# Kernel tuning notes

Hardware: AMD Instinct MI355X
Metric: run time of the kernel (lower is better)

## Reference

```python
import jax, jax.numpy as jnp
import numpy as np

HORIZON = 20
DT = 0.1
EPS = 1e-4
V_MAX = 0.22
W_MAX = 2.8
BATCH = 1048576


def _inv_softplus(v):
    # matches StaticDifferentiableLQR._positive_inverse_softplus
    v = np.clip(np.asarray(v, np.float32) - EPS, 1e-6, None)
    return np.log(np.expm1(v)).astype(np.float32)


def setup_inputs() -> dict:
    key = jax.random.key(0)
    ref = jax.random.normal(key, (BATCH, 5), dtype=jnp.float32)
    return {
        "reference": ref,
        "q_raw": jnp.asarray(_inv_softplus([2.0, 6.0, 4.0])),
        "r_raw": jnp.asarray(_inv_softplus([0.5, 0.8])),
        "qf_raw": jnp.asarray(_inv_softplus([4.0, 10.0, 6.0])),
    }


def _lqr_forward(ref, q_raw, r_raw, qf_raw):
    dtype = ref.dtype
    bsz = ref.shape[0]
    error = ref[:, 0:3]          # [B,3]
    u_ref = ref[:, 3:5]          # [B,2]
    v_ref = u_ref[:, 0]
    w_ref = u_ref[:, 1]

    dt = jnp.asarray(DT, dtype)
    z = jnp.zeros_like(v_ref)
    one = jnp.ones_like(v_ref)
    # Linearized unicycle dynamics A:[B,3,3], B:[B,3,2]
    A = jnp.stack([
        jnp.stack([one, dt * w_ref, z], axis=-1),
        jnp.stack([-dt * w_ref, one, dt * v_ref], axis=-1),
        jnp.stack([z, z, one], axis=-1),
    ], axis=1)
    Bm = jnp.zeros((bsz, 3, 2), dtype).at[:, 0, 0].set(-dt).at[:, 2, 1].set(-dt)

    q = jax.nn.softplus(q_raw) + EPS
    r = jax.nn.softplus(r_raw) + EPS
    qf = jax.nn.softplus(qf_raw) + EPS
    Q = jnp.diag(q).astype(dtype)        # [3,3], broadcasts over batch
    R = jnp.diag(r).astype(dtype)        # [2,2]
    P0 = jnp.broadcast_to(jnp.diag(qf).astype(dtype), (bsz, 3, 3))
    I2 = jnp.eye(2, dtype=dtype)
    K_init = jnp.zeros((bsz, 2, 3), dtype)

    def riccati_step(carry, _):
        P, _ = carry
        BtP = jnp.einsum('bji,bjk->bik', Bm, P)          # B^T P  [B,2,3]
        S = R + BtP @ Bm + EPS * I2                       # [B,2,2]
        K = jnp.linalg.solve(S, BtP @ A)                  # [B,2,3]
        AtP = jnp.einsum('bji,bjk->bik', A, P)            # A^T P  [B,3,3]
        # Q + A^T P A - A^T P B K == Q + A^T P (A - B K)
        P_new = Q + AtP @ (A - Bm @ K)
        return (P_new, K), None

    (_, K0), _ = jax.lax.scan(riccati_step, (P0, K_init), None, length=HORIZON)

    delta_u = -jnp.einsum('bij,bj->bi', K0, error)        # [B,2]
    mean = u_ref + delta_u
    v = jnp.clip(mean[:, 0], -V_MAX, V_MAX)
    w = jnp.clip(mean[:, 1], -W_MAX, W_MAX)
    return jnp.stack([v, w], axis=-1)


def reference(reference, q_raw, r_raw, qf_raw):
    return _lqr_forward(reference, q_raw, r_raw, qf_raw)
```

## Files before the change

### kernel.cpp

```cpp
#include <hip/hip_runtime.h>
#include <math.h>

#define HORIZON 20
#define DT      0.1f
#define EPS     1e-4f
#define V_MAX   0.22f
#define W_MAX   2.8f

#define NQ     57
#define NODES  (NQ * NQ)
#define QHI    4.0f
#define INV_H  ((float)(NQ - 1) / QHI)

#define CAP      65536
#define LIST_OFF 64
#define TBL_OFF  262144

typedef _Float16 h2 __attribute__((ext_vector_type(2)));

__device__ __forceinline__ float softplus_f(float x) {
    return fmaxf(x, 0.0f) + log1pf(expf(-fabsf(x)));
}

__device__ void riccati_K(
    float vref, float wref,
    const float* __restrict__ q_raw, const float* __restrict__ r_raw,
    const float* __restrict__ qf_raw, float K[6])
{
    const float q0  = softplus_f(q_raw[0])  + EPS;
    const float q1  = softplus_f(q_raw[1])  + EPS;
    const float q2  = softplus_f(q_raw[2])  + EPS;
    const float r0e = softplus_f(r_raw[0])  + EPS + EPS;
    const float r1e = softplus_f(r_raw[1])  + EPS + EPS;
    const float qf0 = softplus_f(qf_raw[0]) + EPS;
    const float qf1 = softplus_f(qf_raw[1]) + EPS;
    const float qf2 = softplus_f(qf_raw[2]) + EPS;

    const float dt  = DT;
    const float dt2 = dt * dt;
    const float dtw = dt * wref;
    const float dtv = dt * vref;

    float p00 = qf0, p01 = 0.f, p02 = 0.f, p11 = qf1, p12 = 0.f, p22 = qf2;
    float k00 = 0.f, k01 = 0.f, k02 = 0.f, k10 = 0.f, k11 = 0.f, k12 = 0.f;

    #pragma unroll
    for (int t = 0; t < HORIZON; ++t) {
        const float t00 = p00 - dtw * p01;
        const float t01 = p01 - dtw * p11;
        const float t02 = p02 - dtw * p12;
        const float t10 = dtw * p00 + p01;
        const float t11 = dtw * p01 + p11;
        const float t12 = dtw * p02 + p12;
        const float t20 = dtv * p01 + p02;
        const float t21 = dtv * p11 + p12;
        const float t22 = dtv * p12 + p22;

        const float s00 = r0e + dt2 * p00;
        const float s01 =       dt2 * p02;
        const float s11 = r1e + dt2 * p22;
        const float c = -dt * __builtin_amdgcn_rcpf(s00 * s11 - s01 * s01);
        const float cs11 = c * s11, cs01 = c * s01, cs00 = c * s00;

        k00 = cs11 * t00 - cs01 * t02;
        k01 = cs11 * t10 - cs01 * t12;
        k02 = cs11 * t20 - cs01 * t22;
        k10 = cs00 * t02 - cs01 * t00;
        k11 = cs00 * t12 - cs01 * t10;
        k12 = cs00 * t22 - cs01 * t20;

        const float a00 = 1.0f + dt * k00;
        const float a01 = dtw  + dt * k01;
        const float a02 =        dt * k02;
        const float a20 =        dt * k10;
        const float a21 =        dt * k11;
        const float a22 = 1.0f + dt * k12;

        p00 = q0 + t00 * a00 - t01 * dtw + t02 * a20;
        p01 =      t00 * a01 + t01       + t02 * a21;
        p02 =      t00 * a02 + t01 * dtv + t02 * a22;
        p11 = q1 + t10 * a01 + t11       + t12 * a21;
        p12 =      t10 * a02 + t11 * dtv + t12 * a22;
        p22 = q2 + t20 * a02 + t21 * dtv + t22 * a22;
    }
    K[0] = k00; K[1] = k01; K[2] = k02;
    K[3] = k10; K[4] = k11; K[5] = k12;
}

__device__ __forceinline__ unsigned pack2(float a, float b) {
    h2 h; h[0] = (_Float16)a; h[1] = (_Float16)b;
    return __builtin_bit_cast(unsigned, h);
}

__global__ __launch_bounds__(256) void table_kernel(
    const float* __restrict__ q_raw, const float* __restrict__ r_raw,
    const float* __restrict__ qf_raw, unsigned* __restrict__ ws)
{
    const int idx = blockIdx.x * blockDim.x + threadIdx.x;
    if (idx == 0) ws[0] = 0u;
    if (idx >= NODES) return;
    const int iv = idx % NQ;
    const int iw = idx / NQ;
    const float v = (QHI / (float)(NQ - 1)) * (float)iv;
    const float w = (QHI / (float)(NQ - 1)) * (float)iw;
    float K[6];
    riccati_K(v, w, q_raw, r_raw, qf_raw, K);
    uint4* tbl = reinterpret_cast<uint4*>(ws + TBL_OFF);
    tbl[idx] = make_uint4(pack2(K[0], K[1]), pack2(K[2], K[3]),
                          pack2(K[4], K[5]), 0u);
}

__device__ __forceinline__ float2 eval_one(
    const uint4* __restrict__ nodes,
    float e0, float e1, float e2, float vref, float wref, bool* oor)
{
    const float s1 = (wref < 0.0f) ? -1.0f : 1.0f;
    const float v1 = s1 * vref, w1 = s1 * wref;
    const float e1f = s1 * e1;
    const float s2 = (v1 < 0.0f) ? -1.0f : 1.0f;
    const float vq = s2 * v1;
    const float e2f = s2 * e2;

    *oor = (vq > QHI) | (w1 > QHI);

    float fv = fminf(vq * INV_H, (float)(NQ - 1) - 1e-3f);
    float fw = fminf(w1 * INV_H, (float)(NQ - 1) - 1e-3f);
    const int iv = (int)fv;  const float av = fv - (float)iv;
    const int iw = (int)fw;  const float aw = fw - (float)iw;
    const int b = iw * NQ + iv;

    const uint4 A = nodes[b],      B = nodes[b + 1];
    const uint4 C = nodes[b + NQ], D = nodes[b + NQ + 1];

    const _Float16 hu00 = (_Float16)((1.0f - av) * (1.0f - aw));
    const _Float16 hu01 = (_Float16)(av * (1.0f - aw));
    const _Float16 hu10 = (_Float16)((1.0f - av) * aw);
    const _Float16 hu11 = (_Float16)(av * aw);
    const h2 W00 = {hu00, hu00}, W01 = {hu01, hu01},
             W10 = {hu10, hu10}, W11 = {hu11, hu11};

    #define H2(u) __builtin_bit_cast(h2, u)
    h2 r0 = W00 * H2(A.x) + W01 * H2(B.x) + W10 * H2(C.x) + W11 * H2(D.x);
    h2 r1 = W00 * H2(A.y) + W01 * H2(B.y) + W10 * H2(C.y) + W11 * H2(D.y);
    h2 r2 = W00 * H2(A.z) + W01 * H2(B.z) + W10 * H2(C.z) + W11 * H2(D.z);
    #undef H2

    const float k0 = (float)r0[0], k1 = (float)r0[1];
    const float k2 = (float)r1[0], k3 = (float)r1[1];
    const float k4 = (float)r2[0], k5 = (float)r2[1];

    const float du0 =       k0 * e0 + k1 * e1f + k2 * e2f;
    const float du1 = s2 * (k3 * e0 + k4 * e1f + k5 * e2f);
    const float v = fminf(fmaxf(vref - du0, -V_MAX), V_MAX);
    const float w = fminf(fmaxf(wref - du1, -W_MAX), W_MAX);
    return make_float2(v, w);
}

__global__ __launch_bounds__(512, 4) void lqr_main(
    const float* __restrict__ ref,
    unsigned* __restrict__ ws,
    float* __restrict__ out,
    int batch)
{
    __shared__ uint4 lds[NODES];
    const uint4* gt = reinterpret_cast<const uint4*>(ws + TBL_OFF);
    for (int j = threadIdx.x; j < NODES; j += 512)
        lds[j] = gt[j];
    __syncthreads();

    const int t    = blockIdx.x * 512 + threadIdx.x;
    const int base = 4 * t;
    if (base >= batch) return;

    unsigned* cnt  = ws;
    unsigned* list = ws + LIST_OFF;

    if (base + 3 < batch) {
        const float4* r4 = reinterpret_cast<const float4*>(ref + 5 * base);
        const float4 d0 = r4[0], d1 = r4[1], d2 = r4[2], d3 = r4[3], d4 = r4[4];
        const float r[20] = {d0.x,d0.y,d0.z,d0.w, d1.x,d1.y,d1.z,d1.w,
                             d2.x,d2.y,d2.z,d2.w, d3.x,d3.y,d3.z,d3.w,
                             d4.x,d4.y,d4.z,d4.w};
        bool o0, o1, o2, o3;
        const float2 c0 = eval_one(lds, r[0], r[1], r[2], r[3], r[4], &o0);
        const float2 c1 = eval_one(lds, r[5], r[6], r[7], r[8], r[9], &o1);
        const float2 c2 = eval_one(lds, r[10],r[11],r[12],r[13],r[14], &o2);
        const float2 c3 = eval_one(lds, r[15],r[16],r[17],r[18],r[19], &o3);

        float4* o4 = reinterpret_cast<float4*>(out + 2 * base);
        o4[0] = make_float4(c0.x, c0.y, c1.x, c1.y);
        o4[1] = make_float4(c2.x, c2.y, c3.x, c3.y);

        if (o0) { unsigned p = atomicAdd(cnt, 1u); if (p < CAP) list[p] = base;     }
        if (o1) { unsigned p = atomicAdd(cnt, 1u); if (p < CAP) list[p] = base + 1; }
        if (o2) { unsigned p = atomicAdd(cnt, 1u); if (p < CAP) list[p] = base + 2; }
        if (o3) { unsigned p = atomicAdd(cnt, 1u); if (p < CAP) list[p] = base + 3; }
    } else {
        for (int k = 0; k < 4 && base + k < batch; ++k) {
            const float* r = ref + 5 * (base + k);
            bool oo;
            const float2 c = eval_one(lds, r[0], r[1], r[2], r[3], r[4], &oo);
            out[2 * (base + k)]     = c.x;
            out[2 * (base + k) + 1] = c.y;
            if (oo) { unsigned p = atomicAdd(cnt, 1u); if (p < CAP) list[p] = base + k; }
        }
    }
}

__global__ __launch_bounds__(256) void fixup_kernel(
    const float* __restrict__ ref,
    const unsigned* __restrict__ ws,
    const float* __restrict__ q_raw, const float* __restrict__ r_raw,
    const float* __restrict__ qf_raw,
    float* __restrict__ out)
{
    const unsigned n = min(ws[0], (unsigned)CAP);
    const unsigned* list = ws + LIST_OFF;
    for (unsigned j = threadIdx.x; j < n; j += 256) {
        const unsigned idx = list[j];
        const float e0 = ref[5*idx], e1 = ref[5*idx+1], e2 = ref[5*idx+2];
        const float vr = ref[5*idx+3], wr = ref[5*idx+4];
        float K[6];
        riccati_K(vr, wr, q_raw, r_raw, qf_raw, K);
        const float du0 = K[0]*e0 + K[1]*e1 + K[2]*e2;
        const float du1 = K[3]*e0 + K[4]*e1 + K[5]*e2;
        out[2*idx]   = fminf(fmaxf(vr - du0, -V_MAX), V_MAX);
        out[2*idx+1] = fminf(fmaxf(wr - du1, -W_MAX), W_MAX);
    }
}

extern "C" void kernel_launch(void* const* d_in, const int* in_sizes, int n_in,
                              void* d_out, int out_size, void* d_ws, size_t ws_size,
                              hipStream_t stream) {
    const float* ref    = (const float*)d_in[0];
    const float* q_raw  = (const float*)d_in[1];
    const float* r_raw  = (const float*)d_in[2];
    const float* qf_raw = (const float*)d_in[3];
    float* out = (float*)d_out;
    unsigned* ws = (unsigned*)d_ws;

    const int batch = in_sizes[0] / 5;
    const int quads = (batch + 3) / 4;

    table_kernel<<<(NODES + 255) / 256, 256, 0, stream>>>(q_raw, r_raw, qf_raw, ws);

    const int grid = (quads + 511) / 512;
    lqr_main<<<grid, 512, 0, stream>>>(ref, ws, out, batch);

    fixup_kernel<<<1, 256, 0, stream>>>(ref, ws, q_raw, r_raw, qf_raw, out);
}
```

Measured before the change: 89.23 us.

## Fuse out-of-range fixup into main kernel and overlap ref loads with table staging

Removes the separate single-block fixup kernel and the global atomic list. Threads whose reference falls outside the interpolation table now run the full Riccati recursion inline. The __syncthreads after the table copy into LDS is moved below the ref float4 loads, so global input reads overlap with table staging. This saves a kernel launch, serialized atomics and a one-block tail, at the cost of wave divergence and a larger inlined body that may raise register pressure.

```diff
diff --git a/kernel.cpp b/kernel.cpp
--- a/kernel.cpp
+++ b/kernel.cpp
@@ -12,17 +12,13 @@
 #define QHI    4.0f
 #define INV_H  ((float)(NQ - 1) / QHI)
 
-#define CAP      65536
-#define LIST_OFF 64
-#define TBL_OFF  262144
-
 typedef _Float16 h2 __attribute__((ext_vector_type(2)));
 
 __device__ __forceinline__ float softplus_f(float x) {
     return fmaxf(x, 0.0f) + log1pf(expf(-fabsf(x)));
 }
 
-__device__ void riccati_K(
+__device__ __forceinline__ void riccati_K(
     float vref, float wref,
     const float* __restrict__ q_raw, const float* __restrict__ r_raw,
     const float* __restrict__ qf_raw, float K[6])
@@ -94,10 +90,9 @@
 
 __global__ __launch_bounds__(256) void table_kernel(
     const float* __restrict__ q_raw, const float* __restrict__ r_raw,
-    const float* __restrict__ qf_raw, unsigned* __restrict__ ws)
+    const float* __restrict__ qf_raw, uint4* __restrict__ tbl)
 {
     const int idx = blockIdx.x * blockDim.x + threadIdx.x;
-    if (idx == 0) ws[0] = 0u;
     if (idx >= NODES) return;
     const int iv = idx % NQ;
     const int iw = idx / NQ;
@@ -105,7 +100,6 @@
     const float w = (QHI / (float)(NQ - 1)) * (float)iw;
     float K[6];
     riccati_K(v, w, q_raw, r_raw, qf_raw, K);
-    uint4* tbl = reinterpret_cast<uint4*>(ws + TBL_OFF);
     tbl[idx] = make_uint4(pack2(K[0], K[1]), pack2(K[2], K[3]),
                           pack2(K[4], K[5]), 0u);
 }
@@ -158,26 +152,24 @@
 
 __global__ __launch_bounds__(512, 4) void lqr_main(
     const float* __restrict__ ref,
-    unsigned* __restrict__ ws,
+    const uint4* __restrict__ gt,
+    const float* __restrict__ q_raw, const float* __restrict__ r_raw,
+    const float* __restrict__ qf_raw,
     float* __restrict__ out,
     int batch)
 {
     __shared__ uint4 lds[NODES];
-    const uint4* gt = reinterpret_cast<const uint4*>(ws + TBL_OFF);
     for (int j = threadIdx.x; j < NODES; j += 512)
         lds[j] = gt[j];
-    __syncthreads();
 
     const int t    = blockIdx.x * 512 + threadIdx.x;
     const int base = 4 * t;
-    if (base >= batch) return;
-
-    unsigned* cnt  = ws;
-    unsigned* list = ws + LIST_OFF;
 
     if (base + 3 < batch) {
         const float4* r4 = reinterpret_cast<const float4*>(ref + 5 * base);
         const float4 d0 = r4[0], d1 = r4[1], d2 = r4[2], d3 = r4[3], d4 = r4[4];
+        __syncthreads();
+
         const float r[20] = {d0.x,d0.y,d0.z,d0.w, d1.x,d1.y,d1.z,d1.w,
                              d2.x,d2.y,d2.z,d2.w, d3.x,d3.y,d3.z,d3.w,
                              d4.x,d4.y,d4.z,d4.w};
@@ -191,41 +183,43 @@
         o4[0] = make_float4(c0.x, c0.y, c1.x, c1.y);
         o4[1] = make_float4(c2.x, c2.y, c3.x, c3.y);
 
-        if (o0) { unsigned p = atomicAdd(cnt, 1u); if (p < CAP) list[p] = base;     }
-        if (o1) { unsigned p = atomicAdd(cnt, 1u); if (p < CAP) list[p] = base + 1; }
-        if (o2) { unsigned p = atomicAdd(cnt, 1u); if (p < CAP) list[p] = base + 2; }
-        if (o3) { unsigned p = atomicAdd(cnt, 1u); if (p < CAP) list[p] = base + 3; }
+        if (o0 | o1 | o2 | o3) {
+            const bool oo[4] = {o0, o1, o2, o3};
+            #pragma unroll
+            for (int k = 0; k < 4; ++k) {
+                if (oo[k]) {
+                    const float* rp = ref + 5 * (base + k);
+                    const float e0 = rp[0], e1 = rp[1], e2 = rp[2];
+                    const float vr = rp[3], wr = rp[4];
+                    float K[6];
+                    riccati_K(vr, wr, q_raw, r_raw, qf_raw, K);
+                    const float du0 = K[0]*e0 + K[1]*e1 + K[2]*e2;
+                    const float du1 = K[3]*e0 + K[4]*e1 + K[5]*e2;
+                    out[2*(base+k)]   = fminf(fmaxf(vr - du0, -V_MAX), V_MAX);
+                    out[2*(base+k)+1] = fminf(fmaxf(wr - du1, -W_MAX), W_MAX);
+                }
+            }
+        }
     } else {
-        for (int k = 0; k < 4 && base + k < batch; ++k) {
-            const float* r = ref + 5 * (base + k);
+        __syncthreads();
+        for (int k = 0; k < 4; ++k) {
+            const int idx = base + k;
+            if (idx >= batch) break;
+            const float* rp = ref + 5 * idx;
             bool oo;
-            const float2 c = eval_one(lds, r[0], r[1], r[2], r[3], r[4], &oo);
-            out[2 * (base + k)]     = c.x;
-            out[2 * (base + k) + 1] = c.y;
-            if (oo) { unsigned p = atomicAdd(cnt, 1u); if (p < CAP) list[p] = base + k; }
+            const float2 c = eval_one(lds, rp[0], rp[1], rp[2], rp[3], rp[4], &oo);
+            float vv = c.x, ww = c.y;
+            if (oo) {
+                float K[6];
+                riccati_K(rp[3], rp[4], q_raw, r_raw, qf_raw, K);
+                const float du0 = K[0]*rp[0] + K[1]*rp[1] + K[2]*rp[2];
+                const float du1 = K[3]*rp[0] + K[4]*rp[1] + K[5]*rp[2];
+                vv = fminf(fmaxf(rp[3] - du0, -V_MAX), V_MAX);
+                ww = fminf(fmaxf(rp[4] - du1, -W_MAX), W_MAX);
+            }
+            out[2*idx]   = vv;
+            out[2*idx+1] = ww;
         }
-    }
-}
-
-__global__ __launch_bounds__(256) void fixup_kernel(
-    const float* __restrict__ ref,
-    const unsigned* __restrict__ ws,
-    const float* __restrict__ q_raw, const float* __restrict__ r_raw,
-    const float* __restrict__ qf_raw,
-    float* __restrict__ out)
-{
-    const unsigned n = min(ws[0], (unsigned)CAP);
-    const unsigned* list = ws + LIST_OFF;
-    for (unsigned j = threadIdx.x; j < n; j += 256) {
-        const unsigned idx = list[j];
-        const float e0 = ref[5*idx], e1 = ref[5*idx+1], e2 = ref[5*idx+2];
-        const float vr = ref[5*idx+3], wr = ref[5*idx+4];
-        float K[6];
-        riccati_K(vr, wr, q_raw, r_raw, qf_raw, K);
-        const float du0 = K[0]*e0 + K[1]*e1 + K[2]*e2;
-        const float du1 = K[3]*e0 + K[4]*e1 + K[5]*e2;
-        out[2*idx]   = fminf(fmaxf(vr - du0, -V_MAX), V_MAX);
-        out[2*idx+1] = fminf(fmaxf(wr - du1, -W_MAX), W_MAX);
     }
 }
 
@@ -237,15 +231,13 @@
     const float* r_raw  = (const float*)d_in[2];
     const float* qf_raw = (const float*)d_in[3];
     float* out = (float*)d_out;
-    unsigned* ws = (unsigned*)d_ws;
+    uint4* tbl = (uint4*)d_ws;
 
     const int batch = in_sizes[0] / 5;
     const int quads = (batch + 3) / 4;
 
-    table_kernel<<<(NODES + 255) / 256, 256, 0, stream>>>(q_raw, r_raw, qf_raw, ws);
+    table_kernel<<<(NODES + 255) / 256, 256, 0, stream>>>(q_raw, r_raw, qf_raw, tbl);
 
     const int grid = (quads + 511) / 512;
-    lqr_main<<<grid, 512, 0, stream>>>(ref, ws, out, batch);
-
-    fixup_kernel<<<1, 256, 0, stream>>>(ref, ws, q_raw, r_raw, qf_raw, out);
-}
+    lqr_main<<<grid, 512, 0, stream>>>(ref, tbl, q_raw, r_raw, qf_raw, out, batch);
+}
```

After: 90.38 us. About the same (+1.3%).
